# Kernel tuning notes

Hardware: AMD Instinct MI355X
Metric: run time of the kernel (lower is better)

Reference implementation:

```python
import jax, jax.numpy as jnp
import numpy as np


def cross_scan(x):
    # x: (B, D, H, W) -> xs: (B, 8, D, L)  (row, col, rev-row, rev-col, diag, antidiag, rev-diag, rev-antidiag)
    B, D, H, W = x.shape
    L = H * W
    hs = jnp.arange(H)[:, None]
    ws = jnp.arange(W)[None, :]
    x0 = x.reshape(B, D, L)                          # row-major
    x1 = jnp.swapaxes(x, 2, 3).reshape(B, D, L)      # column-major
    gd = x[:, :, hs, (hs + ws) % W]                  # diagonal gather (B,D,H,W)
    ga = x[:, :, hs, (ws - hs) % W]                  # antidiagonal gather
    x4 = jnp.swapaxes(gd, -1, -2).reshape(B, D, L)
    x5 = jnp.swapaxes(ga, -1, -2).reshape(B, D, L)
    return jnp.stack([x0, x1, x0[..., ::-1], x1[..., ::-1],
                      x4, x5, x4[..., ::-1], x5[..., ::-1]], axis=1)


def cross_merge(ys, H, W):
    # ys: (B, 8, D, L) -> (B, D, L), inverse-scatter + sum of all 8 directions
    B, K, D, L = ys.shape
    hs = jnp.arange(H)[:, None]
    ws = jnp.arange(W)[None, :]
    y = ys[:, 0] + ys[:, 2, :, ::-1]
    yt = (ys[:, 1] + ys[:, 3, :, ::-1]).reshape(B, D, W, H)
    y = y + jnp.swapaxes(yt, -1, -2).reshape(B, D, L)
    # diagonal scatter: result[h, w'] = t[h, (w'-h) % W]
    td = jnp.swapaxes((ys[:, 4] + ys[:, 6, :, ::-1]).reshape(B, D, W, H), -1, -2)
    y = y + td[:, :, hs, (ws - hs) % W].reshape(B, D, L)
    # antidiagonal scatter: result[h, w'] = t[h, (w'+h) % W]
    ta = jnp.swapaxes((ys[:, 5] + ys[:, 7, :, ::-1]).reshape(B, D, W, H), -1, -2)
    y = y + ta[:, :, hs, (ws + hs) % W].reshape(B, D, L)
    return y


def selective_scan(u, delta, A, Bs, Cs, Ds):
    # u, delta: (B, KD, L); A: (KD, N); Bs, Cs: (B, K, N, L); Ds: (KD,)
    Bb, KD, L = u.shape
    K = Bs.shape[1]
    Dh = KD // K
    N = A.shape[1]
    u_ = jnp.moveaxis(u.reshape(Bb, K, Dh, L), -1, 0)        # (L,B,K,Dh)
    d_ = jnp.moveaxis(delta.reshape(Bb, K, Dh, L), -1, 0)
    B_ = jnp.moveaxis(Bs, -1, 0)                              # (L,B,K,N)
    C_ = jnp.moveaxis(Cs, -1, 0)
    A_ = A.reshape(K, Dh, N)

    def step(h, inp):
        u_t, d_t, b_t, c_t = inp
        dA = jnp.exp(d_t[..., None] * A_)                     # (B,K,Dh,N)
        h = h * dA + (d_t * u_t)[..., None] * b_t[:, :, None, :]
        y = jnp.einsum('bkdn,bkn->bkd', h, c_t)
        return h, y

    h0 = jnp.zeros((Bb, K, Dh, N), u.dtype)
    _, ys = jax.lax.scan(step, h0, (u_, d_, B_, C_))          # ys: (L,B,K,Dh)
    ys = jnp.moveaxis(ys, 0, -1).reshape(Bb, KD, L)
    return ys + u * Ds[None, :, None]


def setup_inputs() -> dict:
    key = jax.random.key(0)
    ks = jax.random.split(key, 6)
    B, D, H, W = 2, 192, 64, 64
    K, N, R = 8, 16, 6
    x = jax.random.normal(ks[0], (B, D, H, W), jnp.float32)
    x_proj_weight = jax.random.normal(ks[1], (K, R + 2 * N, D), jnp.float32) * (1.0 / np.sqrt(D))
    dt_projs_weight = jax.random.normal(ks[2], (K, D, R), jnp.float32) * (0.1 / np.sqrt(R))
    dt_projs_bias = jax.random.normal(ks[3], (K, D), jnp.float32) * 0.1
    A_logs = jax.random.uniform(ks[4], (K * D, N), jnp.float32)
    Ds = jax.random.normal(ks[5], (K * D,), jnp.float32)
    ln_w = jnp.ones((D,), jnp.float32)
    ln_b = jnp.zeros((D,), jnp.float32)
    return {"x": x, "x_proj_weight": x_proj_weight, "dt_projs_weight": dt_projs_weight,
            "dt_projs_bias": dt_projs_bias, "A_logs": A_logs, "Ds": Ds,
            "ln_w": ln_w, "ln_b": ln_b}


def reference(x, x_proj_weight, dt_projs_weight, dt_projs_bias, A_logs, Ds, ln_w, ln_b):
    B, D, H, W = x.shape
    K = x_proj_weight.shape[0]
    N = A_logs.shape[1]
    R = dt_projs_weight.shape[2]
    L = H * W
    xs = cross_scan(x)                                            # (B,K,D,L)
    x_dbl = jnp.einsum('bkdl,kcd->bkcl', xs, x_proj_weight)       # (B,K,R+2N,L)
    dts, Bs, Cs = jnp.split(x_dbl, [R, R + N], axis=2)
    dts = jnp.einsum('bkrl,kdr->bkdl', dts, dt_projs_weight)      # (B,K,D,L)
    u = xs.reshape(B, K * D, L)
    delta = jax.nn.softplus(dts.reshape(B, K * D, L) + dt_projs_bias.reshape(1, K * D, 1))
    A = -jnp.exp(A_logs)                                          # (KD,N)
    ys = selective_scan(u, delta, A, Bs, Cs, Ds)                  # (B,KD,L)
    y = cross_merge(ys.reshape(B, K, D, L), H, W)                 # (B,D,L)
    y = jnp.swapaxes(y, 1, 2)                                     # (B,L,D)
    mu = y.mean(-1, keepdims=True)
    var = y.var(-1, keepdims=True)
    y = (y - mu) / jnp.sqrt(var + 1e-5) * ln_w + ln_b             # out_norm (LayerNorm)
    return y.reshape(B, H, W, D)
```

## Files before the change

### kernel.cpp

```cpp
#include <hip/hip_runtime.h>
#include <math.h>

#define BB   2
#define DD   192
#define LL   4096
#define KK   8
#define NN   16
#define RR   6
#define C38  38
#define CPAD 40
#define NCH  64
#define CLEN (LL / NCH)
#define NCHAN (BB * KK * DD)

__device__ __forceinline__ float fexp2(float x) { return __builtin_amdgcn_exp2f(x); }
__device__ __forceinline__ float flog2(float x) { return __builtin_amdgcn_logf(x); }

__device__ __forceinline__ float softplus_f(float x) {
  return fmaxf(x, 0.f) + 0.69314718f * flog2(1.f + fexp2(-1.44269504f * fabsf(x)));
}

__device__ __forceinline__ int src_index(int k, int l) {
  int ll = (k & 2) ? (LL - 1 - l) : l;
  int kb = k & 5;
  if (kb == 0) return ll;
  int h = ll & 63, w = ll >> 6;
  if (kb == 1) return (h << 6) + w;
  if (kb == 4) return (h << 6) + ((h + w) & 63);
  return (h << 6) + ((w - h) & 63);
}

__global__ __launch_bounds__(256) void transpose_x(const float* __restrict__ x,
                                                   float* __restrict__ xT) {
  __shared__ float tile[32][33];
  int b  = blockIdx.z;
  int p0 = blockIdx.x * 32;
  int d0 = blockIdx.y * 32;
  int tx = threadIdx.x, ty = threadIdx.y;
  #pragma unroll
  for (int i = 0; i < 32; i += 8)
    tile[ty + i][tx] = x[((size_t)(b * DD + d0 + ty + i)) * LL + p0 + tx];
  __syncthreads();
  #pragma unroll
  for (int i = 0; i < 32; i += 8)
    xT[((size_t)(b * LL + p0 + ty + i)) * DD + d0 + tx] = tile[tx][ty + i];
}

__global__ __launch_bounds__(256) void proj_kernel(const float* __restrict__ xT,
                                                   const float* __restrict__ W,
                                                   float* __restrict__ xdbl) {
  int k = blockIdx.y, b = blockIdx.z;
  int tx = threadIdx.x;
  int lloc = tx & 127, half = tx >> 7;
  int l = blockIdx.x * 128 + lloc;
  __shared__ __align__(16) float sm[DD * CPAD];
  for (int i = tx; i < C38 * DD; i += 256) {
    int c = i / DD, dq = i - c * DD;
    sm[dq * CPAD + c] = W[(k * C38 + c) * DD + dq];
  }
  for (int dq = tx; dq < DD; dq += 256) { sm[dq * CPAD + 38] = 0.f; sm[dq * CPAD + 39] = 0.f; }
  __syncthreads();

  int p = src_index(k, l);
  const float4* xrow4 = (const float4*)(xT + ((size_t)b * LL + p) * DD) + half * 24;
  const float* wbase = sm + half * 96 * CPAD;
  float4 acc[10];
  #pragma unroll
  for (int c = 0; c < 10; ++c) acc[c] = make_float4(0.f, 0.f, 0.f, 0.f);

  for (int d4 = 0; d4 < 24; ++d4) {
    float4 xv = xrow4[d4];
    #pragma unroll
    for (int s = 0; s < 4; ++s) {
      float xs = (s == 0) ? xv.x : (s == 1) ? xv.y : (s == 2) ? xv.z : xv.w;
      const float4* w4 = (const float4*)(wbase + (d4 * 4 + s) * CPAD);
      #pragma unroll
      for (int c = 0; c < 10; ++c) {
        float4 wv = w4[c];
        acc[c].x = fmaf(wv.x, xs, acc[c].x);
        acc[c].y = fmaf(wv.y, xs, acc[c].y);
        acc[c].z = fmaf(wv.z, xs, acc[c].z);
        acc[c].w = fmaf(wv.w, xs, acc[c].w);
      }
    }
  }
  __syncthreads();
  if (half == 1) {
    float* pr = sm + lloc * 41;
    const float* af = (const float*)acc;
    #pragma unroll
    for (int c = 0; c < 38; ++c) pr[c] = af[c];
  }
  __syncthreads();
  if (half == 0) {
    const float* pr = sm + lloc * 41;
    float* af = (float*)acc;
    #pragma unroll
    for (int c = 0; c < 38; ++c) af[c] += pr[c];
    float* orow = xdbl + ((size_t)((b * KK + k) * LL) + l) * CPAD;
    float4* o4 = (float4*)orow;
    #pragma unroll
    for (int c = 0; c < 9; ++c) o4[c] = acc[c];
    orow[36] = acc[9].x;
    orow[37] = acc[9].y;
  }
}

template <bool FINAL>
__global__ __launch_bounds__(384, 4) void scan_kernel(
    const float* __restrict__ xT, const float* __restrict__ xdbl,
    const float* __restrict__ A_logs, const float* __restrict__ dtw,
    const float* __restrict__ dtb, const float* __restrict__ Ds,
    float* __restrict__ Sarr, float* __restrict__ Qarr, float* __restrict__ Y) {
  constexpr int ROWF  = FINAL ? 40 : 24;
  constexpr int ROWF2 = ROWF / 2;
  constexpr int SRCF2 = FINAL ? 19 : 11;

  __shared__ __align__(16) float rows[CLEN * ROWF];

  const int lane  = threadIdx.x;
  const int ng    = lane >> 5;
  const int dd    = threadIdx.y;
  const int tid   = dd * 64 + lane;
  const int bk    = blockIdx.x;
  const int chunk = blockIdx.y;
  const int b = bk >> 3, k = bk & 7;
  const int d  = dd * 32 + (lane & 31);
  const int kd = k * DD + d;
  const int ch = bk * DD + d;
  const int l0 = chunk * CLEN;

  {
    const float2* src2 = (const float2*)(xdbl + ((size_t)(bk * LL) + l0) * CPAD);
    float2* dst2 = (float2*)rows;
    for (int i = tid; i < CLEN * SRCF2; i += 384) {
      int r = i / SRCF2, c = i - r * SRCF2;
      dst2[r * ROWF2 + c + (c >= 3)] = src2[r * (CPAD / 2) + c];
    }
  }

  float An2[8];
  {
    const float* ap = A_logs + (size_t)kd * NN + ng * 8;
    #pragma unroll
    for (int j = 0; j < 8; ++j) An2[j] = -__expf(ap[j]) * 1.44269504f;
  }
  float wdt[RR];
  #pragma unroll
  for (int r = 0; r < RR; ++r) wdt[r] = dtw[kd * RR + r];
  const float bias = dtb[kd];
  const float dval = FINAL ? Ds[kd] : 0.f;

  float h[8];
  if constexpr (FINAL) {
    const float* h0p = Qarr + ((size_t)chunk * NCHAN + ch) * NN + ng * 8;
    #pragma unroll
    for (int j = 0; j < 8; ++j) h[j] = h0p[j];
  } else {
    #pragma unroll
    for (int j = 0; j < 8; ++j) h[j] = 0.f;
  }

  const float* xTb = xT + (size_t)b * LL * DD + d;
  float S = 0.f;

  __syncthreads();

  auto STEP = [&](int t, int p, float u) {
    const float* row = rows + t * ROWF;
    float dts = bias;
    dts = fmaf(row[0], wdt[0], dts);
    dts = fmaf(row[1], wdt[1], dts);
    dts = fmaf(row[2], wdt[2], dts);
    dts = fmaf(row[3], wdt[3], dts);
    dts = fmaf(row[4], wdt[4], dts);
    dts = fmaf(row[5], wdt[5], dts);
    float spv = softplus_f(dts);
    float du = spv * u;
    const float4* bq = (const float4*)(row + 8 + ng * 8);
    float4 b0 = bq[0], b1 = bq[1];
    float Bvv[8] = {b0.x, b0.y, b0.z, b0.w, b1.x, b1.y, b1.z, b1.w};
    #pragma unroll
    for (int j = 0; j < 8; ++j) {
      float e = fexp2(spv * An2[j]);
      h[j] = fmaf(h[j], e, du * Bvv[j]);
    }
    if constexpr (FINAL) {
      const float4* cq = (const float4*)(row + 24 + ng * 8);
      float4 c0 = cq[0], c1 = cq[1];
      float Cvv[8] = {c0.x, c0.y, c0.z, c0.w, c1.x, c1.y, c1.z, c1.w};
      float y = 0.f;
      #pragma unroll
      for (int j = 0; j < 8; ++j) y = fmaf(h[j], Cvv[j], y);
      y += __shfl_xor(y, 32, 64);
      if (ng == 0) {
        atomicAdd(&Y[(size_t)(b * LL + p) * DD + d], fmaf(u, dval, y));
      }
    } else {
      S += spv;
    }
  };

  int ppA[4], ppB[4];
  float uuA[4], uuB[4];
  #pragma unroll
  for (int s = 0; s < 4; ++s) {
    int p = src_index(k, l0 + s);
    ppA[s] = p; uuA[s] = xTb[(size_t)p * DD];
  }
  for (int tb = 0; tb < CLEN; tb += 8) {
    #pragma unroll
    for (int s = 0; s < 4; ++s) {
      int p = src_index(k, l0 + tb + 4 + s);
      ppB[s] = p; uuB[s] = xTb[(size_t)p * DD];
    }
    #pragma unroll
    for (int s = 0; s < 4; ++s) STEP(tb + s, ppA[s], uuA[s]);
    int nb = (tb + 8 < CLEN) ? tb + 8 : 0;
    #pragma unroll
    for (int s = 0; s < 4; ++s) {
      int p = src_index(k, l0 + nb + s);
      ppA[s] = p; uuA[s] = xTb[(size_t)p * DD];
    }
    #pragma unroll
    for (int s = 0; s < 4; ++s) STEP(tb + 4 + s, ppB[s], uuB[s]);
  }

  if constexpr (!FINAL) {
    if (ng == 0) Sarr[(size_t)chunk * NCHAN + ch] = S;
    float* qp = Qarr + ((size_t)chunk * NCHAN + ch) * NN + ng * 8;
    #pragma unroll
    for (int j = 0; j < 8; ++j) qp[j] = h[j];
  }
}

__global__ __launch_bounds__(256) void stitch_kernel(const float* __restrict__ Sarr,
                                                     float* __restrict__ Qarr,
                                                     const float* __restrict__ A_logs) {
  const int t  = blockIdx.x * 256 + threadIdx.x;
  const int ch = t >> 4, n = t & 15;
  const int kd = ch % (KK * DD);
  const float An2 = -__expf(A_logs[(size_t)kd * NN + n]) * 1.44269504f;

  float q[8], Sv[8];
  #pragma unroll
  for (int i = 0; i < 8; ++i) {
    q[i]  = Qarr[(size_t)i * (NCHAN * NN) + t];
    Sv[i] = Sarr[(size_t)i * NCHAN + ch];
  }
  float h = 0.f;
  for (int cb = 0; cb < NCH; cb += 8) {
    #pragma unroll
    for (int i = 0; i < 8; ++i) {
      const int c = cb + i;
      Qarr[(size_t)c * (NCHAN * NN) + t] = h;
      h = fmaf(fexp2(An2 * Sv[i]), h, q[i]);
      const int cn = c + 8;
      if (cn < NCH) {
        q[i]  = Qarr[(size_t)cn * (NCHAN * NN) + t];
        Sv[i] = Sarr[(size_t)cn * NCHAN + ch];
      }
    }
  }
}

__global__ __launch_bounds__(256) void ln_kernel(const float* __restrict__ Y,
                                                 const float* __restrict__ lw,
                                                 const float* __restrict__ lb,
                                                 float* __restrict__ out) {
  int lane = threadIdx.x & 63;
  int row = blockIdx.x * 4 + (threadIdx.x >> 6);
  const float* yr = Y + (size_t)row * DD;
  float v0 = yr[lane], v1 = yr[lane + 64], v2 = yr[lane + 128];
  float s1 = v0 + v1 + v2;
  float s2 = v0 * v0 + v1 * v1 + v2 * v2;
  #pragma unroll
  for (int m = 32; m >= 1; m >>= 1) {
    s1 += __shfl_xor(s1, m, 64);
    s2 += __shfl_xor(s2, m, 64);
  }
  float mu = s1 * (1.f / DD);
  float var = s2 * (1.f / DD) - mu * mu;
  float inv = rsqrtf(var + 1e-5f);
  float* orow = out + (size_t)row * DD;
  orow[lane]       = (v0 - mu) * inv * lw[lane]       + lb[lane];
  orow[lane + 64]  = (v1 - mu) * inv * lw[lane + 64]  + lb[lane + 64];
  orow[lane + 128] = (v2 - mu) * inv * lw[lane + 128] + lb[lane + 128];
}

extern "C" void kernel_launch(void* const* d_in, const int* in_sizes, int n_in,
                              void* d_out, int out_size, void* d_ws, size_t ws_size,
                              hipStream_t stream) {
  const float* x      = (const float*)d_in[0];
  const float* xpw    = (const float*)d_in[1];
  const float* dtw    = (const float*)d_in[2];
  const float* dtb    = (const float*)d_in[3];
  const float* A_logs = (const float*)d_in[4];
  const float* Ds     = (const float*)d_in[5];
  const float* ln_w   = (const float*)d_in[6];
  const float* ln_b   = (const float*)d_in[7];
  float* out = (float*)d_out;

  float* ws   = (float*)d_ws;
  float* xT   = ws;
  float* xdbl = xT + 1572864;
  float* Y    = xdbl + 2621440;
  float* Sarr = Y + 1572864;
  float* Qarr = Sarr + 196608;

  hipMemsetAsync(Y, 0, 1572864 * sizeof(float), stream);
  transpose_x<<<dim3(LL / 32, DD / 32, BB), dim3(32, 8), 0, stream>>>(x, xT);
  proj_kernel<<<dim3(LL / 128, KK, BB), 256, 0, stream>>>(xT, xpw, xdbl);
  scan_kernel<false><<<dim3(BB * KK, NCH), dim3(64, 6), 0, stream>>>(
      xT, xdbl, A_logs, dtw, dtb, Ds, Sarr, Qarr, Y);
  stitch_kernel<<<(NCHAN * NN) / 256, 256, 0, stream>>>(Sarr, Qarr, A_logs);
  scan_kernel<true><<<dim3(BB * KK, NCH), dim3(64, 6), 0, stream>>>(
      xT, xdbl, A_logs, dtw, dtb, Ds, Sarr, Qarr, Y);
  ln_kernel<<<(BB * LL) / 4, 256, 0, stream>>>(Y, ln_w, ln_b, out);
}
```

Before: 221.8 us.

## Give each scan thread all 16 states and use 128 chunks when workspace allows

Each scan thread now holds all 16 state dimensions for its channel. This removes the two-way split across half-waves, the cross-lane shuffle and the idle half of the lanes on the atomic add, and blocks shrink from 384 to 192 threads. To keep the GPU busy with the smaller blocks, the sequence is cut into 128 chunks when the workspace is large enough, otherwise 64. The trade-off is more registers per thread, possibly lower occupancy, and a longer serial stitch across more chunks.

```diff
diff --git a/kernel.cpp b/kernel.cpp
--- a/kernel.cpp
+++ b/kernel.cpp
@@ -9,8 +9,6 @@
 #define RR   6
 #define C38  38
 #define CPAD 40
-#define NCH  64
-#define CLEN (LL / NCH)
 #define NCHAN (BB * KK * DD)
 
 __device__ __forceinline__ float fexp2(float x) { return __builtin_amdgcn_exp2f(x); }
@@ -106,44 +104,42 @@
   }
 }
 
-template <bool FINAL>
-__global__ __launch_bounds__(384, 4) void scan_kernel(
+template <bool FINAL, int NCHT>
+__global__ __launch_bounds__(192, 4) void scan_kernel(
     const float* __restrict__ xT, const float* __restrict__ xdbl,
     const float* __restrict__ A_logs, const float* __restrict__ dtw,
     const float* __restrict__ dtb, const float* __restrict__ Ds,
     float* __restrict__ Sarr, float* __restrict__ Qarr, float* __restrict__ Y) {
+  constexpr int CLENT = LL / NCHT;
   constexpr int ROWF  = FINAL ? 40 : 24;
   constexpr int ROWF2 = ROWF / 2;
   constexpr int SRCF2 = FINAL ? 19 : 11;
 
-  __shared__ __align__(16) float rows[CLEN * ROWF];
-
-  const int lane  = threadIdx.x;
-  const int ng    = lane >> 5;
-  const int dd    = threadIdx.y;
-  const int tid   = dd * 64 + lane;
+  __shared__ __align__(16) float rows[CLENT * ROWF];
+
+  const int tid   = threadIdx.x;
+  const int d     = tid;
   const int bk    = blockIdx.x;
   const int chunk = blockIdx.y;
   const int b = bk >> 3, k = bk & 7;
-  const int d  = dd * 32 + (lane & 31);
   const int kd = k * DD + d;
   const int ch = bk * DD + d;
-  const int l0 = chunk * CLEN;
+  const int l0 = chunk * CLENT;
 
   {
     const float2* src2 = (const float2*)(xdbl + ((size_t)(bk * LL) + l0) * CPAD);
     float2* dst2 = (float2*)rows;
-    for (int i = tid; i < CLEN * SRCF2; i += 384) {
+    for (int i = tid; i < CLENT * SRCF2; i += 192) {
       int r = i / SRCF2, c = i - r * SRCF2;
       dst2[r * ROWF2 + c + (c >= 3)] = src2[r * (CPAD / 2) + c];
     }
   }
 
-  float An2[8];
+  float An2[NN];
   {
-    const float* ap = A_logs + (size_t)kd * NN + ng * 8;
-    #pragma unroll
-    for (int j = 0; j < 8; ++j) An2[j] = -__expf(ap[j]) * 1.44269504f;
+    const float* ap = A_logs + (size_t)kd * NN;
+    #pragma unroll
+    for (int j = 0; j < NN; ++j) An2[j] = -__expf(ap[j]) * 1.44269504f;
   }
   float wdt[RR];
   #pragma unroll
@@ -151,14 +147,17 @@
   const float bias = dtb[kd];
   const float dval = FINAL ? Ds[kd] : 0.f;
 
-  float h[8];
+  float h[NN];
   if constexpr (FINAL) {
-    const float* h0p = Qarr + ((size_t)chunk * NCHAN + ch) * NN + ng * 8;
-    #pragma unroll
-    for (int j = 0; j < 8; ++j) h[j] = h0p[j];
+    const float4* h0p = (const float4*)(Qarr + ((size_t)chunk * NCHAN + ch) * NN);
+    #pragma unroll
+    for (int j4 = 0; j4 < 4; ++j4) {
+      float4 v = h0p[j4];
+      h[4 * j4 + 0] = v.x; h[4 * j4 + 1] = v.y; h[4 * j4 + 2] = v.z; h[4 * j4 + 3] = v.w;
+    }
   } else {
     #pragma unroll
-    for (int j = 0; j < 8; ++j) h[j] = 0.f;
+    for (int j = 0; j < NN; ++j) h[j] = 0.f;
   }
 
   const float* xTb = xT + (size_t)b * LL * DD + d;
@@ -177,25 +176,36 @@
     dts = fmaf(row[5], wdt[5], dts);
     float spv = softplus_f(dts);
     float du = spv * u;
-    const float4* bq = (const float4*)(row + 8 + ng * 8);
-    float4 b0 = bq[0], b1 = bq[1];
-    float Bvv[8] = {b0.x, b0.y, b0.z, b0.w, b1.x, b1.y, b1.z, b1.w};
-    #pragma unroll
-    for (int j = 0; j < 8; ++j) {
+    float Bvv[NN];
+    #pragma unroll
+    for (int q4 = 0; q4 < 4; ++q4) {
+      float4 v = ((const float4*)(row + 8))[q4];
+      Bvv[4 * q4 + 0] = v.x; Bvv[4 * q4 + 1] = v.y;
+      Bvv[4 * q4 + 2] = v.z; Bvv[4 * q4 + 3] = v.w;
+    }
+    #pragma unroll
+    for (int j = 0; j < NN; ++j) {
       float e = fexp2(spv * An2[j]);
       h[j] = fmaf(h[j], e, du * Bvv[j]);
     }
     if constexpr (FINAL) {
-      const float4* cq = (const float4*)(row + 24 + ng * 8);
-      float4 c0 = cq[0], c1 = cq[1];
-      float Cvv[8] = {c0.x, c0.y, c0.z, c0.w, c1.x, c1.y, c1.z, c1.w};
-      float y = 0.f;
+      float Cvv[NN];
       #pragma unroll
-      for (int j = 0; j < 8; ++j) y = fmaf(h[j], Cvv[j], y);
-      y += __shfl_xor(y, 32, 64);
-      if (ng == 0) {
-        atomicAdd(&Y[(size_t)(b * LL + p) * DD + d], fmaf(u, dval, y));
+      for (int q4 = 0; q4 < 4; ++q4) {
+        float4 v = ((const float4*)(row + 24))[q4];
+        Cvv[4 * q4 + 0] = v.x; Cvv[4 * q4 + 1] = v.y;
+        Cvv[4 * q4 + 2] = v.z; Cvv[4 * q4 + 3] = v.w;
       }
+      float y0 = 0.f, y1 = 0.f, y2 = 0.f, y3 = 0.f;
+      #pragma unroll
+      for (int j = 0; j < NN; j += 4) {
+        y0 = fmaf(h[j + 0], Cvv[j + 0], y0);
+        y1 = fmaf(h[j + 1], Cvv[j + 1], y1);
+        y2 = fmaf(h[j + 2], Cvv[j + 2], y2);
+        y3 = fmaf(h[j + 3], Cvv[j + 3], y3);
+      }
+      float y = (y0 + y1) + (y2 + y3);
+      atomicAdd(&Y[(size_t)(b * LL + p) * DD + d], fmaf(u, dval, y));
     } else {
       S += spv;
     }
@@ -208,7 +218,7 @@
     int p = src_index(k, l0 + s);
     ppA[s] = p; uuA[s] = xTb[(size_t)p * DD];
   }
-  for (int tb = 0; tb < CLEN; tb += 8) {
+  for (int tb = 0; tb < CLENT; tb += 8) {
     #pragma unroll
     for (int s = 0; s < 4; ++s) {
       int p = src_index(k, l0 + tb + 4 + s);
@@ -216,7 +226,7 @@
     }
     #pragma unroll
     for (int s = 0; s < 4; ++s) STEP(tb + s, ppA[s], uuA[s]);
-    int nb = (tb + 8 < CLEN) ? tb + 8 : 0;
+    int nb = (tb + 8 < CLENT) ? tb + 8 : 0;
     #pragma unroll
     for (int s = 0; s < 4; ++s) {
       int p = src_index(k, l0 + nb + s);
@@ -227,13 +237,15 @@
   }
 
   if constexpr (!FINAL) {
-    if (ng == 0) Sarr[(size_t)chunk * NCHAN + ch] = S;
-    float* qp = Qarr + ((size_t)chunk * NCHAN + ch) * NN + ng * 8;
-    #pragma unroll
-    for (int j = 0; j < 8; ++j) qp[j] = h[j];
-  }
-}
-
+    Sarr[(size_t)chunk * NCHAN + ch] = S;
+    float4* qp = (float4*)(Qarr + ((size_t)chunk * NCHAN + ch) * NN);
+    #pragma unroll
+    for (int j4 = 0; j4 < 4; ++j4)
+      qp[j4] = make_float4(h[4 * j4 + 0], h[4 * j4 + 1], h[4 * j4 + 2], h[4 * j4 + 3]);
+  }
+}
+
+template <int NCHT>
 __global__ __launch_bounds__(256) void stitch_kernel(const float* __restrict__ Sarr,
                                                      float* __restrict__ Qarr,
                                                      const float* __restrict__ A_logs) {
@@ -249,14 +261,14 @@
     Sv[i] = Sarr[(size_t)i * NCHAN + ch];
   }
   float h = 0.f;
-  for (int cb = 0; cb < NCH; cb += 8) {
+  for (int cb = 0; cb < NCHT; cb += 8) {
     #pragma unroll
     for (int i = 0; i < 8; ++i) {
       const int c = cb + i;
       Qarr[(size_t)c * (NCHAN * NN) + t] = h;
       h = fmaf(fexp2(An2 * Sv[i]), h, q[i]);
       const int cn = c + 8;
-      if (cn < NCH) {
+      if (cn < NCHT) {
         q[i]  = Qarr[(size_t)cn * (NCHAN * NN) + t];
         Sv[i] = Sarr[(size_t)cn * NCHAN + ch];
       }
@@ -306,15 +318,29 @@
   float* xdbl = xT + 1572864;
   float* Y    = xdbl + 2621440;
   float* Sarr = Y + 1572864;
-  float* Qarr = Sarr + 196608;
 
   hipMemsetAsync(Y, 0, 1572864 * sizeof(float), stream);
   transpose_x<<<dim3(LL / 32, DD / 32, BB), dim3(32, 8), 0, stream>>>(x, xT);
   proj_kernel<<<dim3(LL / 128, KK, BB), 256, 0, stream>>>(xT, xpw, xdbl);
-  scan_kernel<false><<<dim3(BB * KK, NCH), dim3(64, 6), 0, stream>>>(
-      xT, xdbl, A_logs, dtw, dtb, Ds, Sarr, Qarr, Y);
-  stitch_kernel<<<(NCHAN * NN) / 256, 256, 0, stream>>>(Sarr, Qarr, A_logs);
-  scan_kernel<true><<<dim3(BB * KK, NCH), dim3(64, 6), 0, stream>>>(
-      xT, xdbl, A_logs, dtw, dtb, Ds, Sarr, Qarr, Y);
+
+  const size_t base_f  = 1572864 + 2621440 + 1572864;
+  const size_t need128 = (base_f + (size_t)128 * NCHAN * (1 + NN)) * sizeof(float);
+
+  if (ws_size >= need128) {
+    float* Qarr = Sarr + (size_t)128 * NCHAN;
+    scan_kernel<false, 128><<<dim3(BB * KK, 128), 192, 0, stream>>>(
+        xT, xdbl, A_logs, dtw, dtb, Ds, Sarr, Qarr, Y);
+    stitch_kernel<128><<<(NCHAN * NN) / 256, 256, 0, stream>>>(Sarr, Qarr, A_logs);
+    scan_kernel<true, 128><<<dim3(BB * KK, 128), 192, 0, stream>>>(
+        xT, xdbl, A_logs, dtw, dtb, Ds, Sarr, Qarr, Y);
+  } else {
+    float* Qarr = Sarr + (size_t)64 * NCHAN;
+    scan_kernel<false, 64><<<dim3(BB * KK, 64), 192, 0, stream>>>(
+        xT, xdbl, A_logs, dtw, dtb, Ds, Sarr, Qarr, Y);
+    stitch_kernel<64><<<(NCHAN * NN) / 256, 256, 0, stream>>>(Sarr, Qarr, A_logs);
+    scan_kernel<true, 64><<<dim3(BB * KK, 64), 192, 0, stream>>>(
+        xT, xdbl, A_logs, dtw, dtb, Ds, Sarr, Qarr, Y);
+  }
+
   ln_kernel<<<(BB * LL) / 4, 256, 0, stream>>>(Y, ln_w, ln_b, out);
 }
```

After: 233.0 us. 5.0% more time.

## Split proj_kernel work by output channels instead of reduction dimension

Applied to the files above, without the earlier changes.

The projection kernel now has each thread compute 20 output channels for two sequence positions over the full 192-wide reduction, instead of half the reduction for one position and all channels. This removes the shared-memory partial-sum exchange and both extra barriers, and each shared-memory weight load now feeds two positions. Each block covers 256 positions, so the grid is halved. The trade-off is twice as many global x reads per thread, and the two thread halves now read the same x rows.

```diff
diff --git a/kernel.cpp b/kernel.cpp
--- a/kernel.cpp
+++ b/kernel.cpp
@@ -51,8 +51,9 @@
                                                    float* __restrict__ xdbl) {
   int k = blockIdx.y, b = blockIdx.z;
   int tx = threadIdx.x;
-  int lloc = tx & 127, half = tx >> 7;
-  int l = blockIdx.x * 128 + lloc;
+  int slot = tx & 127, chalf = tx >> 7;
+  int l_a = blockIdx.x * 256 + slot;
+  int l_b = l_a + 128;
   __shared__ __align__(16) float sm[DD * CPAD];
   for (int i = tx; i < C38 * DD; i += 256) {
     int c = i / DD, dq = i - c * DD;
@@ -61,49 +62,45 @@
   for (int dq = tx; dq < DD; dq += 256) { sm[dq * CPAD + 38] = 0.f; sm[dq * CPAD + 39] = 0.f; }
   __syncthreads();
 
-  int p = src_index(k, l);
-  const float4* xrow4 = (const float4*)(xT + ((size_t)b * LL + p) * DD) + half * 24;
-  const float* wbase = sm + half * 96 * CPAD;
-  float4 acc[10];
-  #pragma unroll
-  for (int c = 0; c < 10; ++c) acc[c] = make_float4(0.f, 0.f, 0.f, 0.f);
-
-  for (int d4 = 0; d4 < 24; ++d4) {
-    float4 xv = xrow4[d4];
+  int p_a = src_index(k, l_a);
+  int p_b = src_index(k, l_b);
+  const float4* xa4 = (const float4*)(xT + ((size_t)b * LL + p_a) * DD);
+  const float4* xb4 = (const float4*)(xT + ((size_t)b * LL + p_b) * DD);
+  const float* wbase = sm + chalf * 20;
+  float4 accA[5], accB[5];
+  #pragma unroll
+  for (int c = 0; c < 5; ++c) {
+    accA[c] = make_float4(0.f, 0.f, 0.f, 0.f);
+    accB[c] = make_float4(0.f, 0.f, 0.f, 0.f);
+  }
+
+  for (int d4 = 0; d4 < 48; ++d4) {
+    float4 xa = xa4[d4];
+    float4 xb = xb4[d4];
     #pragma unroll
     for (int s = 0; s < 4; ++s) {
-      float xs = (s == 0) ? xv.x : (s == 1) ? xv.y : (s == 2) ? xv.z : xv.w;
+      float xsa = (s == 0) ? xa.x : (s == 1) ? xa.y : (s == 2) ? xa.z : xa.w;
+      float xsb = (s == 0) ? xb.x : (s == 1) ? xb.y : (s == 2) ? xb.z : xb.w;
       const float4* w4 = (const float4*)(wbase + (d4 * 4 + s) * CPAD);
       #pragma unroll
-      for (int c = 0; c < 10; ++c) {
+      for (int c = 0; c < 5; ++c) {
         float4 wv = w4[c];
-        acc[c].x = fmaf(wv.x, xs, acc[c].x);
-        acc[c].y = fmaf(wv.y, xs, acc[c].y);
-        acc[c].z = fmaf(wv.z, xs, acc[c].z);
-        acc[c].w = fmaf(wv.w, xs, acc[c].w);
+        accA[c].x = fmaf(wv.x, xsa, accA[c].x);
+        accA[c].y = fmaf(wv.y, xsa, accA[c].y);
+        accA[c].z = fmaf(wv.z, xsa, accA[c].z);
+        accA[c].w = fmaf(wv.w, xsa, accA[c].w);
+        accB[c].x = fmaf(wv.x, xsb, accB[c].x);
+        accB[c].y = fmaf(wv.y, xsb, accB[c].y);
+        accB[c].z = fmaf(wv.z, xsb, accB[c].z);
+        accB[c].w = fmaf(wv.w, xsb, accB[c].w);
       }
     }
   }
-  __syncthreads();
-  if (half == 1) {
-    float* pr = sm + lloc * 41;
-    const float* af = (const float*)acc;
-    #pragma unroll
-    for (int c = 0; c < 38; ++c) pr[c] = af[c];
-  }
-  __syncthreads();
-  if (half == 0) {
-    const float* pr = sm + lloc * 41;
-    float* af = (float*)acc;
-    #pragma unroll
-    for (int c = 0; c < 38; ++c) af[c] += pr[c];
-    float* orow = xdbl + ((size_t)((b * KK + k) * LL) + l) * CPAD;
-    float4* o4 = (float4*)orow;
-    #pragma unroll
-    for (int c = 0; c < 9; ++c) o4[c] = acc[c];
-    orow[36] = acc[9].x;
-    orow[37] = acc[9].y;
-  }
+
+  float4* oA = (float4*)(xdbl + ((size_t)((b * KK + k) * LL) + l_a) * CPAD + chalf * 20);
+  float4* oB = (float4*)(xdbl + ((size_t)((b * KK + k) * LL) + l_b) * CPAD + chalf * 20);
+  #pragma unroll
+  for (int c = 0; c < 5; ++c) { oA[c] = accA[c]; oB[c] = accB[c]; }
 }
 
 template <bool FINAL>
@@ -310,7 +307,7 @@
 
   hipMemsetAsync(Y, 0, 1572864 * sizeof(float), stream);
   transpose_x<<<dim3(LL / 32, DD / 32, BB), dim3(32, 8), 0, stream>>>(x, xT);
-  proj_kernel<<<dim3(LL / 128, KK, BB), 256, 0, stream>>>(xT, xpw, xdbl);
+  proj_kernel<<<dim3(LL / 256, KK, BB), 256, 0, stream>>>(xT, xpw, xdbl);
   scan_kernel<false><<<dim3(BB * KK, NCH), dim3(64, 6), 0, stream>>>(
       xT, xdbl, A_logs, dtw, dtb, Ds, Sarr, Qarr, Y);
   stitch_kernel<<<(NCHAN * NN) / 256, 256, 0, stream>>>(Sarr, Qarr, A_logs);
```

New measurement: 224.6 us. No clear change (+1.2%).
